# Kernel tuning notes

Measured on AMD Instinct MI355X. Metric: run time of the kernel, lower is better.

The kernel has to match this reference:

```python
import jax, jax.numpy as jnp
import numpy as np

B, T, D_MODEL = 2, 2048, 1024
N_HEAD, D_HEAD = 16, 64
EPS = 1e-5


def setup_inputs() -> dict:
    key = jax.random.key(0)
    ks = jax.random.split(key, 6)
    s = 0.02  # init scale
    x = jax.random.normal(ks[0], (B, T, D_MODEL), jnp.float32)
    Wq = jax.random.normal(ks[1], (D_MODEL, N_HEAD * D_HEAD), jnp.float32) * s
    Wk = jax.random.normal(ks[2], (D_MODEL, N_HEAD * D_HEAD), jnp.float32) * s
    Wv = jax.random.normal(ks[3], (D_MODEL, N_HEAD * D_HEAD), jnp.float32) * s
    Wo = jax.random.normal(ks[4], (N_HEAD * D_HEAD, D_MODEL), jnp.float32) * s
    bo = jnp.zeros((D_MODEL,), jnp.float32)
    gamma = jnp.ones((D_MODEL,), jnp.float32)
    beta = jnp.zeros((D_MODEL,), jnp.float32)
    # causal mask: True = masked out (matches masked_fill semantics)
    mask = jnp.triu(jnp.ones((T, T), dtype=bool), k=1)[None, None]  # [1,1,T,T]
    return {"x": x, "Wq": Wq, "Wk": Wk, "Wv": Wv, "Wo": Wo, "bo": bo,
            "gamma": gamma, "beta": beta, "mask": mask}


def reference(x, Wq, Wk, Wv, Wo, bo, gamma, beta, mask):
    B_, T_, D = x.shape
    # pre-LayerNorm (biased variance, eps=1e-5, matching torch)
    mu = jnp.mean(x, axis=-1, keepdims=True)
    var = jnp.mean(jnp.square(x - mu), axis=-1, keepdims=True)
    xn = (x - mu) / jnp.sqrt(var + EPS) * gamma + beta
    # QKV projections (no bias)
    q = (xn @ Wq).reshape(B_, T_, N_HEAD, D_HEAD)
    k = (xn @ Wk).reshape(B_, T_, N_HEAD, D_HEAD)
    v = (xn @ Wv).reshape(B_, T_, N_HEAD, D_HEAD)
    scale = 1.0 / (D_HEAD ** 0.5)
    scores = jnp.einsum('bthd,bshd->bhts', q, k) * scale  # [B,H,T,T]
    scores = jnp.where(mask, -jnp.finfo(scores.dtype).max, scores)
    attn = jax.nn.softmax(scores, axis=-1)
    o = jnp.einsum('bhts,bshd->bthd', attn, v).reshape(B_, T_, N_HEAD * D_HEAD)
    out = o @ Wo + bo  # dropout is identity (eval / p=0)
    # pre_layernorm=True: residual uses the NORMALIZED x (faithful to source)
    return xn + out
```

## Files before the change

kernel.cpp:

```cpp
#include <hip/hip_runtime.h>
#include <hip/hip_bf16.h>

typedef unsigned short u16;
typedef __attribute__((ext_vector_type(8))) short bf16x8;
typedef __attribute__((ext_vector_type(4))) float f32x4;

typedef unsigned int g_u32 __attribute__((address_space(1)));
typedef unsigned int l_u32 __attribute__((address_space(3)));

#define T_SEQ 2048
#define DM 1024
#define NH 16
#define DH 64

__device__ __forceinline__ float bf2f(u16 u) {
  return __uint_as_float(((unsigned int)u) << 16);
}
__device__ __forceinline__ u16 f2bf(float f) {
  unsigned int u = __float_as_uint(f);
  u += 0x7fff + ((u >> 16) & 1);
  return (u16)(u >> 16);
}
__device__ __forceinline__ bool in_is_f32(const void* gamma) {
  return ((const u16*)gamma)[0] != 0x3F80;
}
__device__ __forceinline__ void gl_lds16(const u16* g, u16* l) {
  __builtin_amdgcn_global_load_lds((g_u32*)g, (l_u32*)l, 16, 0, 0);
}

__global__ __launch_bounds__(256) void ln_k(const void* __restrict__ x,
                                            const void* __restrict__ gamma,
                                            const void* __restrict__ beta,
                                            u16* __restrict__ xn,
                                            float2* __restrict__ stats) {
  bool f32 = in_is_f32(gamma);
  int row = blockIdx.x;
  int t = threadIdx.x;
  float v[4];
  if (f32) {
    float4 u = ((const float4*)((const float*)x + (size_t)row * DM))[t];
    v[0] = u.x; v[1] = u.y; v[2] = u.z; v[3] = u.w;
  } else {
    uint2 u = ((const uint2*)((const u16*)x + (size_t)row * DM))[t];
    v[0] = bf2f((u16)(u.x & 0xffff)); v[1] = bf2f((u16)(u.x >> 16));
    v[2] = bf2f((u16)(u.y & 0xffff)); v[3] = bf2f((u16)(u.y >> 16));
  }
  float s = v[0] + v[1] + v[2] + v[3];
  float ss = v[0]*v[0] + v[1]*v[1] + v[2]*v[2] + v[3]*v[3];
  #pragma unroll
  for (int m = 1; m < 64; m <<= 1) {
    s += __shfl_xor(s, m);
    ss += __shfl_xor(ss, m);
  }
  __shared__ float red[8];
  int wid = t >> 6;
  if ((t & 63) == 0) { red[wid] = s; red[4 + wid] = ss; }
  __syncthreads();
  float S = red[0] + red[1] + red[2] + red[3];
  float SS = red[4] + red[5] + red[6] + red[7];
  float mu = S * (1.0f / DM);
  float var = SS * (1.0f / DM) - mu * mu;
  float rstd = rsqrtf(var + 1e-5f);
  if (t == 0) stats[row] = make_float2(mu, rstd);
  float gv[4], bv[4];
  if (f32) {
    float4 ug = ((const float4*)gamma)[t];
    float4 ub = ((const float4*)beta)[t];
    gv[0] = ug.x; gv[1] = ug.y; gv[2] = ug.z; gv[3] = ug.w;
    bv[0] = ub.x; bv[1] = ub.y; bv[2] = ub.z; bv[3] = ub.w;
  } else {
    uint2 ug = ((const uint2*)gamma)[t];
    uint2 ub = ((const uint2*)beta)[t];
    gv[0] = bf2f((u16)(ug.x & 0xffff)); gv[1] = bf2f((u16)(ug.x >> 16));
    gv[2] = bf2f((u16)(ug.y & 0xffff)); gv[3] = bf2f((u16)(ug.y >> 16));
    bv[0] = bf2f((u16)(ub.x & 0xffff)); bv[1] = bf2f((u16)(ub.x >> 16));
    bv[2] = bf2f((u16)(ub.y & 0xffff)); bv[3] = bf2f((u16)(ub.y >> 16));
  }
  u16 o[4];
  #pragma unroll
  for (int i = 0; i < 4; i++) o[i] = f2bf((v[i] - mu) * rstd * gv[i] + bv[i]);
  uint2 w;
  w.x = (unsigned)o[0] | ((unsigned)o[1] << 16);
  w.y = (unsigned)o[2] | ((unsigned)o[3] << 16);
  *(uint2*)&xn[(size_t)row * DM + t * 4] = w;
}

__global__ __launch_bounds__(256) void transp_cvt(const void* __restrict__ W0,
                                                  const void* __restrict__ W1,
                                                  const void* __restrict__ W2,
                                                  u16* __restrict__ out,
                                                  const void* __restrict__ gamma) {
  bool f32 = in_is_f32(gamma);
  int z = blockIdx.z;
  const void* in = (z == 0) ? W0 : (z == 1) ? W1 : W2;
  u16* dst0 = out + (size_t)z * 1024 * 1024;
  __shared__ __align__(16) u16 tile[64][72];
  int c0 = blockIdx.x * 64, r0 = blockIdx.y * 64;
  int t = threadIdx.x;
  int rr = t >> 2, seg = t & 3;
  u16 w[16];
  if (f32) {
    const float4* p = (const float4*)((const float*)in + (size_t)(r0 + rr) * 1024 + c0 + seg * 16);
    float4 q0 = p[0], q1 = p[1], q2 = p[2], q3 = p[3];
    w[0] = f2bf(q0.x);  w[1] = f2bf(q0.y);  w[2] = f2bf(q0.z);  w[3] = f2bf(q0.w);
    w[4] = f2bf(q1.x);  w[5] = f2bf(q1.y);  w[6] = f2bf(q1.z);  w[7] = f2bf(q1.w);
    w[8] = f2bf(q2.x);  w[9] = f2bf(q2.y);  w[10] = f2bf(q2.z); w[11] = f2bf(q2.w);
    w[12] = f2bf(q3.x); w[13] = f2bf(q3.y); w[14] = f2bf(q3.z); w[15] = f2bf(q3.w);
  } else {
    const u16* p = (const u16*)in + (size_t)(r0 + rr) * 1024 + c0 + seg * 16;
    bf16x8 a0 = *(const bf16x8*)p;
    bf16x8 a1 = *(const bf16x8*)(p + 8);
    #pragma unroll
    for (int i = 0; i < 8; i++) { w[i] = (u16)a0[i]; w[8 + i] = (u16)a1[i]; }
  }
  #pragma unroll
  for (int i = 0; i < 16; i++) tile[rr][seg * 16 + i] = w[i];
  __syncthreads();
  u16 vals[16];
  #pragma unroll
  for (int i = 0; i < 16; i++) vals[i] = tile[seg * 16 + i][rr];
  u16* dst = &dst0[(size_t)(c0 + rr) * 1024 + r0 + seg * 16];
  #pragma unroll
  for (int q = 0; q < 4; q++) {
    ushort4 p4;
    p4.x = vals[4 * q]; p4.y = vals[4 * q + 1]; p4.z = vals[4 * q + 2]; p4.w = vals[4 * q + 3];
    *(ushort4*)(dst + 4 * q) = p4;
  }
}

__global__ __launch_bounds__(256) void gemm128(const u16* __restrict__ A,
                                               const u16* __restrict__ BT,
                                               u16* __restrict__ Cq,
                                               u16* __restrict__ vt,
                                               void* __restrict__ Cout,
                                               const void* __restrict__ bo,
                                               const void* __restrict__ x,
                                               const void* __restrict__ gamma,
                                               const void* __restrict__ beta,
                                               const float2* __restrict__ stats,
                                               int mode) {
  __shared__ __align__(16) u16 As[128 * 32];
  __shared__ __align__(16) u16 Bs[128 * 32];
  const int K = 1024;
  int tid = threadIdx.x;
  int lane = tid & 63, wid = tid >> 6;
  int wm = wid >> 1, wn = wid & 1;
  int m0 = blockIdx.x * 128, n0 = blockIdx.y * 128;
  int quad = lane >> 4, lcol = lane & 15;
  bool vmode = (mode == 0) && (n0 >= 2048);

  f32x4 acc[4][4];
  #pragma unroll
  for (int i = 0; i < 4; i++)
    #pragma unroll
    for (int j = 0; j < 4; j++) acc[i][j] = (f32x4){0.f, 0.f, 0.f, 0.f};

  int srow = lane >> 2, scol = (lane & 3) * 8;
  const u16* Ag = A + (size_t)(m0 + wid * 16 + srow) * K + scol;
  const u16* Bg = BT + (size_t)(n0 + wid * 16 + srow) * K + scol;
  u16* AsW = As + wid * 16 * 32;
  u16* BsW = Bs + wid * 16 * 32;

  for (int k0 = 0; k0 < K; k0 += 32) {
    gl_lds16(Ag + k0, AsW);
    gl_lds16(Ag + (size_t)64 * K + k0, AsW + 64 * 32);
    gl_lds16(Bg + k0, BsW);
    gl_lds16(Bg + (size_t)64 * K + k0, BsW + 64 * 32);
    __syncthreads();
    bf16x8 af[4], bfr[4];
    #pragma unroll
    for (int i = 0; i < 4; i++)
      af[i] = *(const bf16x8*)&As[(wm * 64 + i * 16 + lcol) * 32 + quad * 8];
    #pragma unroll
    for (int j = 0; j < 4; j++)
      bfr[j] = *(const bf16x8*)&Bs[(wn * 64 + j * 16 + lcol) * 32 + quad * 8];
    if (vmode) {
      #pragma unroll
      for (int i = 0; i < 4; i++)
        #pragma unroll
        for (int j = 0; j < 4; j++)
          acc[i][j] = __builtin_amdgcn_mfma_f32_16x16x32_bf16(af[i], bfr[j], acc[i][j], 0, 0, 0);
    } else {
      #pragma unroll
      for (int i = 0; i < 4; i++)
        #pragma unroll
        for (int j = 0; j < 4; j++)
          acc[i][j] = __builtin_amdgcn_mfma_f32_16x16x32_bf16(bfr[j], af[i], acc[i][j], 0, 0, 0);
    }
    __syncthreads();
  }

  if (mode == 0) {
    if (n0 < 2048) {
      #pragma unroll
      for (int i = 0; i < 4; i++) {
        int m = m0 + wm * 64 + i * 16 + lcol;
        #pragma unroll
        for (int j = 0; j < 4; j++) {
          int nb = n0 + wn * 64 + j * 16 + quad * 4;
          ushort4 p;
          p.x = f2bf(acc[i][j][0]); p.y = f2bf(acc[i][j][1]);
          p.z = f2bf(acc[i][j][2]); p.w = f2bf(acc[i][j][3]);
          *(ushort4*)&Cq[(size_t)m * 2048 + nb] = p;
        }
      }
    } else {
      #pragma unroll
      for (int i = 0; i < 4; i++)
        #pragma unroll
        for (int j = 0; j < 4; j++) {
          int c = n0 - 2048 + wn * 64 + j * 16 + lcol;
          int h = c >> 6, d = c & 63;
          int tb = m0 + wm * 64 + i * 16 + quad * 4;
          int bb = tb >> 11, tt = tb & 2047;
          ushort4 p;
          p.x = f2bf(acc[i][j][0]); p.y = f2bf(acc[i][j][1]);
          p.z = f2bf(acc[i][j][2]); p.w = f2bf(acc[i][j][3]);
          *(ushort4*)&vt[((size_t)(bb * NH + h) * DH + d) * T_SEQ + tt] = p;
        }
    }
  } else {
    bool f32 = in_is_f32(gamma);
    #pragma unroll
    for (int i = 0; i < 4; i++) {
      int m = m0 + wm * 64 + i * 16 + lcol;
      float2 st = stats[m];
      #pragma unroll
      for (int j = 0; j < 4; j++) {
        int nb = n0 + wn * 64 + j * 16 + quad * 4;
        size_t idx = (size_t)m * DM + nb;
        float g4[4], b4[4], bo4[4], x4[4];
        if (f32) {
          float4 g = *(const float4*)((const float*)gamma + nb);
          float4 be = *(const float4*)((const float*)beta + nb);
          float4 bb = *(const float4*)((const float*)bo + nb);
          float4 xv = *(const float4*)((const float*)x + idx);
          g4[0]=g.x; g4[1]=g.y; g4[2]=g.z; g4[3]=g.w;
          b4[0]=be.x; b4[1]=be.y; b4[2]=be.z; b4[3]=be.w;
          bo4[0]=bb.x; bo4[1]=bb.y; bo4[2]=bb.z; bo4[3]=bb.w;
          x4[0]=xv.x; x4[1]=xv.y; x4[2]=xv.z; x4[3]=xv.w;
        } else {
          const u16* gp = (const u16*)gamma + nb;
          const u16* bp = (const u16*)beta + nb;
          const u16* op = (const u16*)bo + nb;
          const u16* xp = (const u16*)x + idx;
          #pragma unroll
          for (int r = 0; r < 4; r++) {
            g4[r] = bf2f(gp[r]); b4[r] = bf2f(bp[r]);
            bo4[r] = bf2f(op[r]); x4[r] = bf2f(xp[r]);
          }
        }
        float o4[4];
        #pragma unroll
        for (int r = 0; r < 4; r++) {
          float xnv = (x4[r] - st.x) * st.y * g4[r] + b4[r];
          o4[r] = acc[i][j][r] + bo4[r] + xnv;
        }
        if (f32) {
          float4 o; o.x = o4[0]; o.y = o4[1]; o.z = o4[2]; o.w = o4[3];
          *(float4*)((float*)Cout + idx) = o;
        } else {
          ushort4 o;
          o.x = f2bf(o4[0]); o.y = f2bf(o4[1]); o.z = f2bf(o4[2]); o.w = f2bf(o4[3]);
          *(ushort4*)((u16*)Cout + idx) = o;
        }
      }
    }
  }
}

__global__ __launch_bounds__(256) void attn(const u16* __restrict__ qk,
                                            const u16* __restrict__ vt,
                                            u16* __restrict__ o) {
  __shared__ __align__(16) u16 Ks[64 * 72];
  __shared__ __align__(16) u16 Vs[64 * 72];
  __shared__ __align__(16) u16 Psm[4][16 * 72];
  int tid = threadIdx.x;
  int lane = tid & 63, wid = tid >> 6;
  int bh = blockIdx.y;
  int b = bh >> 4, h = bh & 15;
  int quad = lane >> 4, lcol = lane & 15;
  int r0 = tid >> 3, seg8 = (tid & 7) * 8;

  const u16* Kbase = qk + (size_t)(b * T_SEQ) * 2048 + 1024 + h * DH;
  const u16* Vbase = vt + (size_t)(b * NH + h) * DH * T_SEQ;

  #pragma unroll
  for (int pi = 0; pi < 2; pi++) {
    int qt = pi ? (int)blockIdx.x : 31 - (int)blockIdx.x;
    int q0 = qt * 64 + wid * 16;
    const u16* qrow = qk + ((size_t)(b * T_SEQ) + q0 + lcol) * 2048 + h * DH + quad * 8;
    bf16x8 qa0 = *(const bf16x8*)(qrow);
    bf16x8 qa1 = *(const bf16x8*)(qrow + 32);

    f32x4 Oacc[4];
    #pragma unroll
    for (int jd = 0; jd < 4; jd++) Oacc[jd] = (f32x4){0.f, 0.f, 0.f, 0.f};
    float lpart[4] = {0.f, 0.f, 0.f, 0.f};
    int ktmax = qt * 64;

    uint4 kp0 = *(const uint4*)(Kbase + (size_t)r0 * 2048 + seg8);
    uint4 kp1 = *(const uint4*)(Kbase + (size_t)(r0 + 32) * 2048 + seg8);
    uint4 vp0 = *(const uint4*)(Vbase + (size_t)r0 * 2048 + seg8);
    uint4 vp1 = *(const uint4*)(Vbase + (size_t)(r0 + 32) * 2048 + seg8);

    for (int kt = 0; kt <= ktmax; kt += 64) {
      __syncthreads();
      *(uint4*)&Ks[r0 * 72 + seg8] = kp0;
      *(uint4*)&Ks[(r0 + 32) * 72 + seg8] = kp1;
      *(uint4*)&Vs[r0 * 72 + seg8] = vp0;
      *(uint4*)&Vs[(r0 + 32) * 72 + seg8] = vp1;
      __syncthreads();
      if (kt < ktmax) {
        int kn = kt + 64;
        kp0 = *(const uint4*)(Kbase + (size_t)(kn + r0) * 2048 + seg8);
        kp1 = *(const uint4*)(Kbase + (size_t)(kn + r0 + 32) * 2048 + seg8);
        vp0 = *(const uint4*)(Vbase + (size_t)r0 * 2048 + kn + seg8);
        vp1 = *(const uint4*)(Vbase + (size_t)(r0 + 32) * 2048 + kn + seg8);
      }
      f32x4 S[4];
      #pragma unroll
      for (int j = 0; j < 4; j++) {
        bf16x8 kb0 = *(const bf16x8*)&Ks[(j * 16 + lcol) * 72 + quad * 8];
        bf16x8 kb1 = *(const bf16x8*)&Ks[(j * 16 + lcol) * 72 + 32 + quad * 8];
        f32x4 s = (f32x4){0.f, 0.f, 0.f, 0.f};
        s = __builtin_amdgcn_mfma_f32_16x16x32_bf16(qa0, kb0, s, 0, 0, 0);
        s = __builtin_amdgcn_mfma_f32_16x16x32_bf16(qa1, kb1, s, 0, 0, 0);
        S[j] = s;
      }
      if (kt < ktmax) {
        #pragma unroll
        for (int r = 0; r < 4; r++) {
          float rs = 0.f;
          #pragma unroll
          for (int j = 0; j < 4; j++) {
            float p = __expf(S[j][r] * 0.125f);
            S[j][r] = p;
            rs += p;
          }
          lpart[r] += rs;
        }
      } else {
        #pragma unroll
        for (int r = 0; r < 4; r++) {
          int qg = q0 + quad * 4 + r;
          float rs = 0.f;
          #pragma unroll
          for (int j = 0; j < 4; j++) {
            int key = kt + j * 16 + lcol;
            float p = (key <= qg) ? __expf(S[j][r] * 0.125f) : 0.f;
            S[j][r] = p;
            rs += p;
          }
          lpart[r] += rs;
        }
      }
      #pragma unroll
      for (int j = 0; j < 4; j++)
        #pragma unroll
        for (int r = 0; r < 4; r++)
          Psm[wid][(quad * 4 + r) * 72 + j * 16 + lcol] = f2bf(S[j][r]);
      #pragma unroll
      for (int s = 0; s < 2; s++) {
        bf16x8 pa = *(const bf16x8*)&Psm[wid][lcol * 72 + s * 32 + quad * 8];
        #pragma unroll
        for (int jd = 0; jd < 4; jd++) {
          bf16x8 vb = *(const bf16x8*)&Vs[(jd * 16 + lcol) * 72 + s * 32 + quad * 8];
          Oacc[jd] = __builtin_amdgcn_mfma_f32_16x16x32_bf16(pa, vb, Oacc[jd], 0, 0, 0);
        }
      }
    }
    #pragma unroll
    for (int r = 0; r < 4; r++) {
      float rs = lpart[r];
      rs += __shfl_xor(rs, 1);
      rs += __shfl_xor(rs, 2);
      rs += __shfl_xor(rs, 4);
      rs += __shfl_xor(rs, 8);
      float inv = 1.0f / rs;
      int qg = q0 + quad * 4 + r;
      size_t rowbase = ((size_t)(b * T_SEQ) + qg) * DM + h * DH;
      #pragma unroll
      for (int jd = 0; jd < 4; jd++)
        o[rowbase + jd * 16 + lcol] = f2bf(Oacc[jd][r] * inv);
    }
  }
}

extern "C" void kernel_launch(void* const* d_in, const int* in_sizes, int n_in,
                              void* d_out, int out_size, void* d_ws, size_t ws_size,
                              hipStream_t stream) {
  (void)in_sizes; (void)n_in; (void)out_size; (void)ws_size;
  const void* x     = d_in[0];
  const void* Wq    = d_in[1];
  const void* Wk    = d_in[2];
  const void* Wv    = d_in[3];
  const void* Wo    = d_in[4];
  const void* bo    = d_in[5];
  const void* gamma = d_in[6];
  const void* beta  = d_in[7];

  u16* ws = (u16*)d_ws;
  u16* xn   = ws;
  u16* qkb  = xn + (size_t)4096 * 1024;
  u16* vt   = qkb + (size_t)4096 * 2048;
  u16* obWT = vt + (size_t)2 * 16 * 64 * 2048;
  float2* stats = (float2*)(obWT + (size_t)4096 * 1024);
  u16* WT  = obWT;
  u16* WoT = xn;

  ln_k<<<4096, 256, 0, stream>>>(x, gamma, beta, xn, stats);

  transp_cvt<<<dim3(16, 16, 3), 256, 0, stream>>>(Wq, Wk, Wv, WT, gamma);

  gemm128<<<dim3(32, 24), 256, 0, stream>>>(xn, WT, qkb, vt, nullptr,
                                            nullptr, nullptr, gamma, nullptr,
                                            nullptr, 0);

  transp_cvt<<<dim3(16, 16, 1), 256, 0, stream>>>(Wo, Wo, Wo, WoT, gamma);

  attn<<<dim3(16, 32), 256, 0, stream>>>(qkb, vt, obWT);

  gemm128<<<dim3(32, 8), 256, 0, stream>>>(obWT, WoT, nullptr, nullptr,
                                           d_out, bo, x, gamma, beta, stats, 1);
}
```

Before: 243.3 us.

## Double-buffer LDS in GEMM and attention, shrink output-projection tile to 64 rows

Both GEMMs now load the next K-slice from global memory into registers while the current slice is consumed from a second LDS buffer. This replaces direct global-to-LDS loads and cuts the per-step barriers from two to one. The attention kernel gets the same register-prefetch ping-pong LDS scheme for its K/V tiles. The output-projection GEMM uses a 64-row tile, doubling its block count to 512 to fill more CUs. The cost is double the LDS footprint and more registers for prefetched data, which can lower occupancy.

```diff
diff --git a/kernel.cpp b/kernel.cpp
--- a/kernel.cpp
+++ b/kernel.cpp
@@ -4,9 +4,6 @@
 typedef unsigned short u16;
 typedef __attribute__((ext_vector_type(8))) short bf16x8;
 typedef __attribute__((ext_vector_type(4))) float f32x4;
-
-typedef unsigned int g_u32 __attribute__((address_space(1)));
-typedef unsigned int l_u32 __attribute__((address_space(3)));
 
 #define T_SEQ 2048
 #define DM 1024
@@ -24,8 +21,9 @@
 __device__ __forceinline__ bool in_is_f32(const void* gamma) {
   return ((const u16*)gamma)[0] != 0x3F80;
 }
-__device__ __forceinline__ void gl_lds16(const u16* g, u16* l) {
-  __builtin_amdgcn_global_load_lds((g_u32*)g, (l_u32*)l, 16, 0, 0);
+__device__ __forceinline__ void barrier_lgkm() {
+  __builtin_amdgcn_s_waitcnt(0xC07F);
+  __builtin_amdgcn_s_barrier();
 }
 
 __global__ __launch_bounds__(256) void ln_k(const void* __restrict__ x,
@@ -128,7 +126,8 @@
   }
 }
 
-__global__ __launch_bounds__(256) void gemm128(const u16* __restrict__ A,
+template<int TM>
+__global__ __launch_bounds__(256) void gemm_db(const u16* __restrict__ A,
                                                const u16* __restrict__ BT,
                                                u16* __restrict__ Cq,
                                                u16* __restrict__ vt,
@@ -139,79 +138,107 @@
                                                const void* __restrict__ beta,
                                                const float2* __restrict__ stats,
                                                int mode) {
-  __shared__ __align__(16) u16 As[128 * 32];
-  __shared__ __align__(16) u16 Bs[128 * 32];
+  constexpr int NI = (TM == 128) ? 4 : 1;
+  constexpr int NJ = (TM == 128) ? 4 : 8;
+  constexpr int ACH = (TM == 128) ? 2 : 1;
+  __shared__ __align__(16) u16 As[2][TM * 32];
+  __shared__ __align__(16) u16 Bs[2][128 * 32];
   const int K = 1024;
   int tid = threadIdx.x;
   int lane = tid & 63, wid = tid >> 6;
-  int wm = wid >> 1, wn = wid & 1;
-  int m0 = blockIdx.x * 128, n0 = blockIdx.y * 128;
+  int wm = (TM == 128) ? (wid >> 1) : wid;
+  int wn = (TM == 128) ? (wid & 1) : 0;
+  int m0 = blockIdx.x * TM, n0 = blockIdx.y * 128;
   int quad = lane >> 4, lcol = lane & 15;
   bool vmode = (mode == 0) && (n0 >= 2048);
 
-  f32x4 acc[4][4];
-  #pragma unroll
-  for (int i = 0; i < 4; i++)
-    #pragma unroll
-    for (int j = 0; j < 4; j++) acc[i][j] = (f32x4){0.f, 0.f, 0.f, 0.f};
-
-  int srow = lane >> 2, scol = (lane & 3) * 8;
-  const u16* Ag = A + (size_t)(m0 + wid * 16 + srow) * K + scol;
-  const u16* Bg = BT + (size_t)(n0 + wid * 16 + srow) * K + scol;
-  u16* AsW = As + wid * 16 * 32;
-  u16* BsW = Bs + wid * 16 * 32;
-
+  f32x4 acc[NI][NJ];
+  #pragma unroll
+  for (int i = 0; i < NI; i++)
+    #pragma unroll
+    for (int j = 0; j < NJ; j++) acc[i][j] = (f32x4){0.f, 0.f, 0.f, 0.f};
+
+  int srow = tid >> 2, scol = (tid & 3) * 8;
+  const u16* Ag = A + (size_t)(m0 + srow) * K + scol;
+  const u16* Bg = BT + (size_t)(n0 + srow) * K + scol;
+
+  #pragma unroll
+  for (int c = 0; c < ACH; c++)
+    *(uint4*)(&As[0][0] + c * 2048 + tid * 8) = *(const uint4*)(Ag + (size_t)c * 64 * K);
+  #pragma unroll
+  for (int c = 0; c < 2; c++)
+    *(uint4*)(&Bs[0][0] + c * 2048 + tid * 8) = *(const uint4*)(Bg + (size_t)c * 64 * K);
+
+  int cur = 0;
   for (int k0 = 0; k0 < K; k0 += 32) {
-    gl_lds16(Ag + k0, AsW);
-    gl_lds16(Ag + (size_t)64 * K + k0, AsW + 64 * 32);
-    gl_lds16(Bg + k0, BsW);
-    gl_lds16(Bg + (size_t)64 * K + k0, BsW + 64 * 32);
-    __syncthreads();
-    bf16x8 af[4], bfr[4];
-    #pragma unroll
-    for (int i = 0; i < 4; i++)
-      af[i] = *(const bf16x8*)&As[(wm * 64 + i * 16 + lcol) * 32 + quad * 8];
-    #pragma unroll
-    for (int j = 0; j < 4; j++)
-      bfr[j] = *(const bf16x8*)&Bs[(wn * 64 + j * 16 + lcol) * 32 + quad * 8];
+    barrier_lgkm();
+    bool more = (k0 + 32) < K;
+    uint4 na[ACH], nb[2];
+    if (more) {
+      #pragma unroll
+      for (int c = 0; c < ACH; c++)
+        na[c] = *(const uint4*)(Ag + (size_t)c * 64 * K + k0 + 32);
+      #pragma unroll
+      for (int c = 0; c < 2; c++)
+        nb[c] = *(const uint4*)(Bg + (size_t)c * 64 * K + k0 + 32);
+    }
+    bf16x8 af[NI], bfr[NJ];
+    #pragma unroll
+    for (int i = 0; i < NI; i++) {
+      int row = (TM == 128) ? (wm * 64 + i * 16 + lcol) : (wm * 16 + lcol);
+      af[i] = *(const bf16x8*)&As[cur][row * 32 + quad * 8];
+    }
+    #pragma unroll
+    for (int j = 0; j < NJ; j++) {
+      int col = ((TM == 128) ? wn * 64 : 0) + j * 16 + lcol;
+      bfr[j] = *(const bf16x8*)&Bs[cur][col * 32 + quad * 8];
+    }
     if (vmode) {
       #pragma unroll
-      for (int i = 0; i < 4; i++)
-        #pragma unroll
-        for (int j = 0; j < 4; j++)
+      for (int i = 0; i < NI; i++)
+        #pragma unroll
+        for (int j = 0; j < NJ; j++)
           acc[i][j] = __builtin_amdgcn_mfma_f32_16x16x32_bf16(af[i], bfr[j], acc[i][j], 0, 0, 0);
     } else {
       #pragma unroll
-      for (int i = 0; i < 4; i++)
-        #pragma unroll
-        for (int j = 0; j < 4; j++)
+      for (int i = 0; i < NI; i++)
+        #pragma unroll
+        for (int j = 0; j < NJ; j++)
           acc[i][j] = __builtin_amdgcn_mfma_f32_16x16x32_bf16(bfr[j], af[i], acc[i][j], 0, 0, 0);
     }
-    __syncthreads();
+    if (more) {
+      #pragma unroll
+      for (int c = 0; c < ACH; c++)
+        *(uint4*)(&As[cur ^ 1][0] + c * 2048 + tid * 8) = na[c];
+      #pragma unroll
+      for (int c = 0; c < 2; c++)
+        *(uint4*)(&Bs[cur ^ 1][0] + c * 2048 + tid * 8) = nb[c];
+    }
+    cur ^= 1;
   }
 
   if (mode == 0) {
-    if (n0 < 2048) {
-      #pragma unroll
-      for (int i = 0; i < 4; i++) {
-        int m = m0 + wm * 64 + i * 16 + lcol;
-        #pragma unroll
-        for (int j = 0; j < 4; j++) {
-          int nb = n0 + wn * 64 + j * 16 + quad * 4;
+    if (!vmode) {
+      #pragma unroll
+      for (int i = 0; i < NI; i++) {
+        int m = m0 + ((TM == 128) ? wm * 64 + i * 16 : wm * 16) + lcol;
+        #pragma unroll
+        for (int j = 0; j < NJ; j++) {
+          int nb2 = n0 + ((TM == 128) ? wn * 64 : 0) + j * 16 + quad * 4;
           ushort4 p;
           p.x = f2bf(acc[i][j][0]); p.y = f2bf(acc[i][j][1]);
           p.z = f2bf(acc[i][j][2]); p.w = f2bf(acc[i][j][3]);
-          *(ushort4*)&Cq[(size_t)m * 2048 + nb] = p;
+          *(ushort4*)&Cq[(size_t)m * 2048 + nb2] = p;
         }
       }
     } else {
       #pragma unroll
-      for (int i = 0; i < 4; i++)
-        #pragma unroll
-        for (int j = 0; j < 4; j++) {
-          int c = n0 - 2048 + wn * 64 + j * 16 + lcol;
+      for (int i = 0; i < NI; i++)
+        #pragma unroll
+        for (int j = 0; j < NJ; j++) {
+          int c = n0 - 2048 + ((TM == 128) ? wn * 64 : 0) + j * 16 + lcol;
           int h = c >> 6, d = c & 63;
-          int tb = m0 + wm * 64 + i * 16 + quad * 4;
+          int tb = m0 + ((TM == 128) ? wm * 64 + i * 16 : wm * 16) + quad * 4;
           int bb = tb >> 11, tt = tb & 2047;
           ushort4 p;
           p.x = f2bf(acc[i][j][0]); p.y = f2bf(acc[i][j][1]);
@@ -222,27 +249,27 @@
   } else {
     bool f32 = in_is_f32(gamma);
     #pragma unroll
-    for (int i = 0; i < 4; i++) {
-      int m = m0 + wm * 64 + i * 16 + lcol;
+    for (int i = 0; i < NI; i++) {
+      int m = m0 + ((TM == 128) ? wm * 64 + i * 16 : wm * 16) + lcol;
       float2 st = stats[m];
       #pragma unroll
-      for (int j = 0; j < 4; j++) {
-        int nb = n0 + wn * 64 + j * 16 + quad * 4;
-        size_t idx = (size_t)m * DM + nb;
+      for (int j = 0; j < NJ; j++) {
+        int nb2 = n0 + ((TM == 128) ? wn * 64 : 0) + j * 16 + quad * 4;
+        size_t idx = (size_t)m * DM + nb2;
         float g4[4], b4[4], bo4[4], x4[4];
         if (f32) {
-          float4 g = *(const float4*)((const float*)gamma + nb);
-          float4 be = *(const float4*)((const float*)beta + nb);
-          float4 bb = *(const float4*)((const float*)bo + nb);
+          float4 g = *(const float4*)((const float*)gamma + nb2);
+          float4 be = *(const float4*)((const float*)beta + nb2);
+          float4 bb = *(const float4*)((const float*)bo + nb2);
           float4 xv = *(const float4*)((const float*)x + idx);
           g4[0]=g.x; g4[1]=g.y; g4[2]=g.z; g4[3]=g.w;
           b4[0]=be.x; b4[1]=be.y; b4[2]=be.z; b4[3]=be.w;
           bo4[0]=bb.x; bo4[1]=bb.y; bo4[2]=bb.z; bo4[3]=bb.w;
           x4[0]=xv.x; x4[1]=xv.y; x4[2]=xv.z; x4[3]=xv.w;
         } else {
-          const u16* gp = (const u16*)gamma + nb;
-          const u16* bp = (const u16*)beta + nb;
-          const u16* op = (const u16*)bo + nb;
+          const u16* gp = (const u16*)gamma + nb2;
+          const u16* bp = (const u16*)beta + nb2;
+          const u16* op = (const u16*)bo + nb2;
           const u16* xp = (const u16*)x + idx;
           #pragma unroll
           for (int r = 0; r < 4; r++) {
@@ -272,8 +299,8 @@
 __global__ __launch_bounds__(256) void attn(const u16* __restrict__ qk,
                                             const u16* __restrict__ vt,
                                             u16* __restrict__ o) {
-  __shared__ __align__(16) u16 Ks[64 * 72];
-  __shared__ __align__(16) u16 Vs[64 * 72];
+  __shared__ __align__(16) u16 Ks[2][64 * 72];
+  __shared__ __align__(16) u16 Vs[2][64 * 72];
   __shared__ __align__(16) u16 Psm[4][16 * 72];
   int tid = threadIdx.x;
   int lane = tid & 63, wid = tid >> 6;
@@ -303,15 +330,17 @@
     uint4 kp1 = *(const uint4*)(Kbase + (size_t)(r0 + 32) * 2048 + seg8);
     uint4 vp0 = *(const uint4*)(Vbase + (size_t)r0 * 2048 + seg8);
     uint4 vp1 = *(const uint4*)(Vbase + (size_t)(r0 + 32) * 2048 + seg8);
-
+    barrier_lgkm();
+    *(uint4*)&Ks[0][r0 * 72 + seg8] = kp0;
+    *(uint4*)&Ks[0][(r0 + 32) * 72 + seg8] = kp1;
+    *(uint4*)&Vs[0][r0 * 72 + seg8] = vp0;
+    *(uint4*)&Vs[0][(r0 + 32) * 72 + seg8] = vp1;
+
+    int cur = 0;
     for (int kt = 0; kt <= ktmax; kt += 64) {
-      __syncthreads();
-      *(uint4*)&Ks[r0 * 72 + seg8] = kp0;
-      *(uint4*)&Ks[(r0 + 32) * 72 + seg8] = kp1;
-      *(uint4*)&Vs[r0 * 72 + seg8] = vp0;
-      *(uint4*)&Vs[(r0 + 32) * 72 + seg8] = vp1;
-      __syncthreads();
-      if (kt < ktmax) {
+      barrier_lgkm();
+      bool more = kt < ktmax;
+      if (more) {
         int kn = kt + 64;
         kp0 = *(const uint4*)(Kbase + (size_t)(kn + r0) * 2048 + seg8);
         kp1 = *(const uint4*)(Kbase + (size_t)(kn + r0 + 32) * 2048 + seg8);
@@ -321,14 +350,14 @@
       f32x4 S[4];
       #pragma unroll
       for (int j = 0; j < 4; j++) {
-        bf16x8 kb0 = *(const bf16x8*)&Ks[(j * 16 + lcol) * 72 + quad * 8];
-        bf16x8 kb1 = *(const bf16x8*)&Ks[(j * 16 + lcol) * 72 + 32 + quad * 8];
+        bf16x8 kb0 = *(const bf16x8*)&Ks[cur][(j * 16 + lcol) * 72 + quad * 8];
+        bf16x8 kb1 = *(const bf16x8*)&Ks[cur][(j * 16 + lcol) * 72 + 32 + quad * 8];
         f32x4 s = (f32x4){0.f, 0.f, 0.f, 0.f};
         s = __builtin_amdgcn_mfma_f32_16x16x32_bf16(qa0, kb0, s, 0, 0, 0);
         s = __builtin_amdgcn_mfma_f32_16x16x32_bf16(qa1, kb1, s, 0, 0, 0);
         S[j] = s;
       }
-      if (kt < ktmax) {
+      if (more) {
         #pragma unroll
         for (int r = 0; r < 4; r++) {
           float rs = 0.f;
@@ -365,10 +394,17 @@
         bf16x8 pa = *(const bf16x8*)&Psm[wid][lcol * 72 + s * 32 + quad * 8];
         #pragma unroll
         for (int jd = 0; jd < 4; jd++) {
-          bf16x8 vb = *(const bf16x8*)&Vs[(jd * 16 + lcol) * 72 + s * 32 + quad * 8];
+          bf16x8 vb = *(const bf16x8*)&Vs[cur][(jd * 16 + lcol) * 72 + s * 32 + quad * 8];
           Oacc[jd] = __builtin_amdgcn_mfma_f32_16x16x32_bf16(pa, vb, Oacc[jd], 0, 0, 0);
         }
       }
+      if (more) {
+        *(uint4*)&Ks[cur ^ 1][r0 * 72 + seg8] = kp0;
+        *(uint4*)&Ks[cur ^ 1][(r0 + 32) * 72 + seg8] = kp1;
+        *(uint4*)&Vs[cur ^ 1][r0 * 72 + seg8] = vp0;
+        *(uint4*)&Vs[cur ^ 1][(r0 + 32) * 72 + seg8] = vp1;
+      }
+      cur ^= 1;
     }
     #pragma unroll
     for (int r = 0; r < 4; r++) {
@@ -413,14 +449,14 @@
 
   transp_cvt<<<dim3(16, 16, 3), 256, 0, stream>>>(Wq, Wk, Wv, WT, gamma);
 
-  gemm128<<<dim3(32, 24), 256, 0, stream>>>(xn, WT, qkb, vt, nullptr,
-                                            nullptr, nullptr, gamma, nullptr,
-                                            nullptr, 0);
+  gemm_db<128><<<dim3(32, 24), 256, 0, stream>>>(xn, WT, qkb, vt, nullptr,
+                                                 nullptr, nullptr, gamma, nullptr,
+                                                 nullptr, 0);
 
   transp_cvt<<<dim3(16, 16, 1), 256, 0, stream>>>(Wo, Wo, Wo, WoT, gamma);
 
   attn<<<dim3(16, 32), 256, 0, stream>>>(qkb, vt, obWT);
 
-  gemm128<<<dim3(32, 8), 256, 0, stream>>>(obWT, WoT, nullptr, nullptr,
-                                           d_out, bo, x, gamma, beta, stats, 1);
-}
+  gemm_db<64><<<dim3(64, 8), 256, 0, stream>>>(obWT, WoT, nullptr, nullptr,
+                                               d_out, bo, x, gamma, beta, stats, 1);
+}
```

Measured after the change: 349.2 us. 1.44x slower.
